# Kernel optimization log

Measured on AMD Instinct MI355X. Metric: run time of the kernel, lower is better.

The kernel has to match this reference:

```python
import jax, jax.numpy as jnp
import numpy as np

N = 50000      # nodes
E = 1600000    # edges (before self loops)
F = 128        # input_dim
H = 4          # num_heads
D = 32         # hidden_dim (per head)
B = 16         # graphs in batch
NEG_SLOPE = 0.2  # PyG GATv2Conv default negative_slope


def setup_inputs() -> dict:
    key = jax.random.key(0)
    ks = jax.random.split(key, 8)
    x = jax.random.normal(ks[0], (N, F), dtype=jnp.float32)
    edge_index = jax.random.randint(ks[1], (2, E), 0, N, dtype=jnp.int32)
    batch = jnp.sort(jax.random.randint(ks[2], (N,), 0, B, dtype=jnp.int32))
    s = 0.05
    W_l = jax.random.normal(ks[3], (F, H * D), dtype=jnp.float32) * s
    b_l = jnp.zeros((H * D,), dtype=jnp.float32)
    W_r = jax.random.normal(ks[4], (F, H * D), dtype=jnp.float32) * s
    b_r = jnp.zeros((H * D,), dtype=jnp.float32)
    att = jax.random.normal(ks[5], (H, D), dtype=jnp.float32) * s
    bias = jnp.zeros((H * D,), dtype=jnp.float32)
    return {"x": x, "edge_index": edge_index, "batch": batch,
            "W_l": W_l, "b_l": b_l, "W_r": W_r, "b_r": b_r,
            "att": att, "bias": bias}


def reference(x, edge_index, batch, W_l, b_l, W_r, b_r, att, bias):
    n = x.shape[0]
    # PyG GATv2Conv adds self loops by default
    loops = jnp.arange(n, dtype=edge_index.dtype)
    src = jnp.concatenate([edge_index[0], loops])  # message source j
    dst = jnp.concatenate([edge_index[1], loops])  # message target i

    xl = (x @ W_l + b_l).reshape(n, H, D)  # source transform
    xr = (x @ W_r + b_r).reshape(n, H, D)  # target transform

    # per-edge GATv2 attention logits: a^T LeakyReLU(xl_j + xr_i)
    m = xl[src] + xr[dst]                                   # [E+N, H, D]
    e = jnp.sum(jax.nn.leaky_relu(m, NEG_SLOPE) * att, -1)  # [E+N, H]

    # softmax over incoming edges of each destination node
    e_max = jax.ops.segment_max(e, dst, num_segments=n)
    ex = jnp.exp(e - e_max[dst])
    den = jax.ops.segment_sum(ex, dst, num_segments=n)
    alpha = ex / den[dst]                                   # [E+N, H]

    # weighted scatter-sum aggregation of source features
    out = jax.ops.segment_sum(alpha[..., None] * xl[src], dst, num_segments=n)
    out = out.reshape(n, H * D) + bias                      # concat heads + bias
    out = jax.nn.relu(out)

    # global max pool over nodes of each graph
    pooled = jax.ops.segment_max(out, batch, num_segments=B)
    pooled = jnp.where(jnp.isfinite(pooled), pooled, 0.0)   # guard empty graphs
    return pooled
```

## Files before the change

kernel.cpp:

```cpp
#include <hip/hip_runtime.h>

#define NN 50000
#define NE 1600000
#define FDIM 128
#define CDIM 128
#define NGRAPH 16
#define SLOPE 0.2f
#define CSTRIDE 96
#define BINSH 7
#define NBIN 391
#define EPB 6400
#define NB1 250
#define EPT 25
#define CAP 5120
#define POOL_NODES 64
#define POOL_NB ((NN + POOL_NODES - 1) / POOL_NODES)
#define TNB 782

__device__ __forceinline__ unsigned short f2bf(float f) {
    unsigned u = __float_as_uint(f);
    return (unsigned short)((u + 0x7FFFu + ((u >> 16) & 1u)) >> 16);
}
__device__ __forceinline__ unsigned packbf(float a, float b) {
    return (unsigned)f2bf(a) | ((unsigned)f2bf(b) << 16);
}
__device__ __forceinline__ unsigned short f2h(float f) {
    union { _Float16 h; unsigned short u; } c;
    c.h = (_Float16)f;
    return c.u;
}

typedef __attribute__((ext_vector_type(8))) short short8;
typedef __attribute__((ext_vector_type(4))) float f32x4;
typedef _Float16 h2 __attribute__((ext_vector_type(2)));
union FragU { uint4 u; short8 s; };
union HU    { uint4 u; h2 h[4]; };

__global__ __launch_bounds__(256) void k_init(float* __restrict__ out,
                                              int* __restrict__ gbin_cnt) {
    int i = blockIdx.x * 256 + threadIdx.x;
    if (i < NGRAPH * CDIM) out[i] = 0.f;
    if (i < NBIN) gbin_cnt[i] = 0;
}

__global__ __launch_bounds__(256) void k_front(
    const float* __restrict__ x,
    const float* __restrict__ Wl, const float* __restrict__ bl,
    const float* __restrict__ Wr, const float* __restrict__ br,
    const int* __restrict__ src, const int* __restrict__ dst,
    int* __restrict__ gbin_cnt, unsigned* __restrict__ gstage,
    unsigned short* __restrict__ xlh, unsigned short* __restrict__ xrh) {
    __shared__ __align__(16) char shraw[32768];
    const int tid = threadIdx.x;

    if (blockIdx.x < NB1) {
        int* bcnt = (int*)shraw;
        int* boff = bcnt + NBIN;
        int* gb   = boff + NBIN;
        int* sc   = gb + NBIN;
        unsigned* st = (unsigned*)(sc + 256);
        const int t  = tid;
        const int e0 = blockIdx.x * EPB;

        for (int b = t; b < NBIN; b += 256) bcnt[b] = 0;
        __syncthreads();

        unsigned sd[EPT]; int bn[EPT]; int pl[EPT];
#pragma unroll
        for (int k = 0; k < EPT; k++) {
            int e = e0 + k * 256 + t;
            int s = src[e], d = dst[e];
            bn[k] = d >> BINSH;
            sd[k] = (unsigned)s | ((unsigned)(d & 127) << 16)
                                | ((unsigned)bn[k] << 23);
            pl[k] = atomicAdd(&bcnt[bn[k]], 1);
        }
        __syncthreads();

        int c0 = (2*t     < NBIN) ? bcnt[2*t]     : 0;
        int c1 = (2*t + 1 < NBIN) ? bcnt[2*t + 1] : 0;
        int v  = c0 + c1;
        sc[t] = v; __syncthreads();
        for (int off = 1; off < 256; off <<= 1) {
            int add = (t >= off) ? sc[t - off] : 0;
            __syncthreads();
            sc[t] += add;
            __syncthreads();
        }
        int base = sc[t] - v;
        if (2*t     < NBIN) boff[2*t]     = base;
        if (2*t + 1 < NBIN) boff[2*t + 1] = base + c0;
        __syncthreads();

        for (int b = t; b < NBIN; b += 256) {
            int c = bcnt[b];
            gb[b] = (c > 0) ? atomicAdd(&gbin_cnt[b], c) : 0;
        }
#pragma unroll
        for (int k = 0; k < EPT; k++) st[boff[bn[k]] + pl[k]] = sd[k];
        __syncthreads();

        for (int idx = t; idx < EPB; idx += 256) {
            unsigned w = st[idx];
            int b = w >> 23;
            int p = gb[b] + (idx - boff[b]);
            if (p < CAP) gstage[(size_t)b * CAP + p] = w;
        }
    } else {
        uint4* wfrag = (uint4*)shraw;
        const int bid   = blockIdx.x - NB1;
        const int wv    = tid >> 6;
        const int lane  = tid & 63;
        const int quad  = lane >> 4;
        const int col   = lane & 15;
        const int node0 = bid * 64;
        const int nodeA = node0 + wv * 16 + col;
        const bool aval = nodeA < NN;

        FragU afrag[4];
#pragma unroll
        for (int kq = 0; kq < 4; kq++) {
            float4 lo = make_float4(0.f,0.f,0.f,0.f), hi = lo;
            if (aval) {
                const float* ap = &x[(size_t)nodeA * FDIM + kq * 32 + quad * 8];
                lo = *(const float4*)ap;
                hi = *(const float4*)(ap + 4);
            }
            afrag[kq].u.x = packbf(lo.x, lo.y);
            afrag[kq].u.y = packbf(lo.z, lo.w);
            afrag[kq].u.z = packbf(hi.x, hi.y);
            afrag[kq].u.w = packbf(hi.z, hi.w);
        }

        const int myrow0 = node0 + wv * 16 + quad * 4;

        for (int mat = 0; mat < 2; mat++) {
            const float* W  = mat ? Wr : Wl;
            const float* bb = mat ? br : bl;
            unsigned short* dsto = mat ? xrh : xlh;
            __syncthreads();
            for (int i = 0; i < 8; i++) {
                int C = i * 256 + tid;
                int ccol = C & 15, cq = (C >> 4) & 3, ckq = (C >> 6) & 3, cnt_ = C >> 8;
                const float* wp = &W[(size_t)(ckq * 32 + cq * 8) * CDIM + cnt_ * 16 + ccol];
                uint4 u;
                u.x = packbf(wp[0],        wp[CDIM]);
                u.y = packbf(wp[2*CDIM],   wp[3*CDIM]);
                u.z = packbf(wp[4*CDIM],   wp[5*CDIM]);
                u.w = packbf(wp[6*CDIM],   wp[7*CDIM]);
                wfrag[C] = u;
            }
            __syncthreads();

#pragma unroll
            for (int nt = 0; nt < 8; nt++) {
                f32x4 acc = {0.f, 0.f, 0.f, 0.f};
#pragma unroll
                for (int kq = 0; kq < 4; kq++) {
                    FragU bfr;
                    bfr.u = wfrag[(nt * 4 + kq) * 64 + lane];
                    acc = __builtin_amdgcn_mfma_f32_16x16x32_bf16(
                              afrag[kq].s, bfr.s, acc, 0, 0, 0);
                }
                int ch = nt * 16 + col;
                float bv = bb[ch];
#pragma unroll
                for (int r = 0; r < 4; r++) {
                    int node = myrow0 + r;
                    if (node < NN)
                        dsto[(size_t)node * CDIM + ch] = f2h(acc[r] + bv);
                }
            }
        }
    }
}

__global__ __launch_bounds__(512) void k_csr(
    const int* __restrict__ gbin_cnt, const unsigned* __restrict__ gstage,
    int* __restrict__ cnt, unsigned short* __restrict__ colp) {
    __shared__ int nfill[128];
    __shared__ unsigned short crow[128 * CSTRIDE];
    const int bin = blockIdx.x;
    const int t   = threadIdx.x;
    const int n0  = bin << BINSH;
    const int nb  = min(128, NN - n0);
    const int m   = min(gbin_cnt[bin], CAP);

    if (t < 128) nfill[t] = 0;
    __syncthreads();

    unsigned w[10];
    bool     ok[10];
#pragma unroll
    for (int k = 0; k < 10; k++) {
        int i = k * 512 + t;
        ok[k] = i < m;
        if (ok[k]) w[k] = gstage[(size_t)bin * CAP + i];
    }
#pragma unroll
    for (int k = 0; k < 10; k++) {
        if (ok[k]) {
            int dl = (w[k] >> 16) & 127;
            int p  = atomicAdd(&nfill[dl], 1);
            if (p < CSTRIDE - 1)
                crow[dl * CSTRIDE + p] = (unsigned short)(w[k] & 0xFFFF);
        }
    }
    __syncthreads();

    if (t < nb) {
        int c = min(nfill[t], CSTRIDE - 1);
        crow[t * CSTRIDE + c] = (unsigned short)(n0 + t);
        cnt[n0 + t] = c + 1;
    }
    __syncthreads();

    unsigned* gout = (unsigned*)colp + (size_t)bin * (128 * CSTRIDE / 2);
    const unsigned* cin = (const unsigned*)crow;
    for (int idx = t; idx < 128 * CSTRIDE / 2; idx += 512) gout[idx] = cin[idx];
}

__device__ __forceinline__ void edge_body(
    const char* __restrict__ xlb, unsigned chb, int j,
    const h2* __restrict__ rx, const h2* __restrict__ ah,
    float& s, float* __restrict__ acc) {
    HU q;
    q.u = *(const uint4*)(xlb + (((unsigned)j << 8) | chb));
    const h2 c02 = {(_Float16)SLOPE, (_Float16)SLOPE};
    float d = 0.f;
#pragma unroll
    for (int k = 0; k < 4; k++) {
        h2 t  = q.h[k] + rx[k];
        h2 lk = __builtin_elementwise_max(t, t * c02);
#if __has_builtin(__builtin_amdgcn_fdot2)
        d = __builtin_amdgcn_fdot2(lk, ah[k], d, false);
#else
        d = fmaf((float)lk.x, (float)ah[k].x, d);
        d = fmaf((float)lk.y, (float)ah[k].y, d);
#endif
    }
    d += __shfl_xor(d, 1);
    d += __shfl_xor(d, 2);
    float w = __expf(d);
    s += w;
#pragma unroll
    for (int k = 0; k < 4; k++) {
        acc[2*k]   = fmaf(w, (float)q.h[k].x, acc[2*k]);
        acc[2*k+1] = fmaf(w, (float)q.h[k].y, acc[2*k+1]);
    }
}

__global__ __launch_bounds__(256) void k_aggregate(
    const unsigned short* __restrict__ xlh, const unsigned short* __restrict__ xrh,
    const float* __restrict__ att, const float* __restrict__ bias,
    const int* __restrict__ cnt, const unsigned short* __restrict__ colp,
    float* __restrict__ nodeout) {
    const int wave = blockIdx.x * 4 + (threadIdx.x >> 6);
    const int lane = threadIdx.x & 63;
    const int i     = wave;
    const size_t start = (size_t)i * CSTRIDE;
    const int deg   = cnt[i];
    const int grp   = lane >> 4;
    const int ch0   = (lane & 15) * 8;
    const unsigned chb = (unsigned)(ch0 * 2);
    const char* xlb = (const char*)xlh;

    int cj0 = (int)colp[start + lane];
    int cj1 = 0;
    if (deg > 64) cj1 = (int)colp[start + 64 + lane];

    HU rxu;
    rxu.u = *(const uint4*)&xrh[(size_t)i * CDIM + ch0];
    const float4 aa0 = *(const float4*)&att[ch0];
    const float4 aa1 = *(const float4*)&att[ch0 + 4];
    h2 ah[4];
    ah[0] = h2{(_Float16)aa0.x, (_Float16)aa0.y};
    ah[1] = h2{(_Float16)aa0.z, (_Float16)aa0.w};
    ah[2] = h2{(_Float16)aa1.x, (_Float16)aa1.y};
    ah[3] = h2{(_Float16)aa1.z, (_Float16)aa1.w};

    float s = 0.f;
    float acc[8];
#pragma unroll
    for (int k = 0; k < 8; k++) acc[k] = 0.f;

    const int full = deg >> 2;
    const int f0   = full < 16 ? full : 16;
#pragma unroll 2
    for (int t = 0; t < f0; t++) {
        int j = __shfl(cj0, t * 4 + grp);
        edge_body(xlb, chb, j, rxu.h, ah, s, acc);
    }
    for (int t = 16; t < full; t++) {
        int j = __shfl(cj1, t * 4 + grp - 64);
        edge_body(xlb, chb, j, rxu.h, ah, s, acc);
    }
    int e  = full * 4 + grp;
    int jt = (e < 64) ? __shfl(cj0, e) : __shfl(cj1, (e - 64) & 63);
    if (e < deg)
        edge_body(xlb, chb, jt, rxu.h, ah, s, acc);

#pragma unroll
    for (int dist = 16; dist <= 32; dist <<= 1) {
        s += __shfl_xor(s, dist);
#pragma unroll
        for (int k = 0; k < 8; k++) acc[k] += __shfl_xor(acc[k], dist);
    }

    if (grp == 0) {
        float inv = 1.f / s;
        float4 o0, o1;
        const float4 b0 = *(const float4*)&bias[ch0];
        const float4 b1 = *(const float4*)&bias[ch0 + 4];
        o0.x = fmaxf(fmaf(acc[0], inv, b0.x), 0.f);
        o0.y = fmaxf(fmaf(acc[1], inv, b0.y), 0.f);
        o0.z = fmaxf(fmaf(acc[2], inv, b0.z), 0.f);
        o0.w = fmaxf(fmaf(acc[3], inv, b0.w), 0.f);
        o1.x = fmaxf(fmaf(acc[4], inv, b1.x), 0.f);
        o1.y = fmaxf(fmaf(acc[5], inv, b1.y), 0.f);
        o1.z = fmaxf(fmaf(acc[6], inv, b1.z), 0.f);
        o1.w = fmaxf(fmaf(acc[7], inv, b1.w), 0.f);
        float* op = &nodeout[(size_t)i * CDIM + ch0];
        *(float4*)op       = o0;
        *(float4*)(op + 4) = o1;
    }
}

__global__ __launch_bounds__(256) void k_pool(
    const float* __restrict__ nodeout, const int* __restrict__ batch,
    float* __restrict__ out) {
    const int tid  = threadIdx.x;
    const int c4   = (tid & 31) * 4;
    const int nl   = tid >> 5;
    const int base = blockIdx.x * POOL_NODES;
    float4 mx = make_float4(0.f, 0.f, 0.f, 0.f);
    int cur = -1;
#pragma unroll
    for (int k = 0; k < POOL_NODES / 8; k++) {
        int node = base + k * 8 + nl;
        if (node >= NN) break;
        int g = batch[node];
        if (g != cur) {
            if (cur >= 0) {
                int* op = (int*)&out[cur * CDIM + c4];
                if (mx.x > 0.f) atomicMax(op,     __float_as_int(mx.x));
                if (mx.y > 0.f) atomicMax(op + 1, __float_as_int(mx.y));
                if (mx.z > 0.f) atomicMax(op + 2, __float_as_int(mx.z));
                if (mx.w > 0.f) atomicMax(op + 3, __float_as_int(mx.w));
            }
            cur = g;
            mx = make_float4(0.f, 0.f, 0.f, 0.f);
        }
        float4 v = *(const float4*)&nodeout[(size_t)node * CDIM + c4];
        mx.x = fmaxf(mx.x, v.x);
        mx.y = fmaxf(mx.y, v.y);
        mx.z = fmaxf(mx.z, v.z);
        mx.w = fmaxf(mx.w, v.w);
    }
    if (cur >= 0) {
        int* op = (int*)&out[cur * CDIM + c4];
        if (mx.x > 0.f) atomicMax(op,     __float_as_int(mx.x));
        if (mx.y > 0.f) atomicMax(op + 1, __float_as_int(mx.y));
        if (mx.z > 0.f) atomicMax(op + 2, __float_as_int(mx.z));
        if (mx.w > 0.f) atomicMax(op + 3, __float_as_int(mx.w));
    }
}

extern "C" void kernel_launch(void* const* d_in, const int* in_sizes, int n_in,
                              void* d_out, int out_size, void* d_ws, size_t ws_size,
                              hipStream_t stream) {
    const float* x     = (const float*)d_in[0];
    const int*   ei    = (const int*)d_in[1];
    const int*   batch = (const int*)d_in[2];
    const float* Wl    = (const float*)d_in[3];
    const float* bl    = (const float*)d_in[4];
    const float* Wr    = (const float*)d_in[5];
    const float* br    = (const float*)d_in[6];
    const float* att   = (const float*)d_in[7];
    const float* bias  = (const float*)d_in[8];
    float* out = (float*)d_out;

    char* w = (char*)d_ws;
    float*          nodeout  = (float*)w;          w += (size_t)NN * CDIM * 4;
    unsigned short* xlh      = (unsigned short*)w; w += (size_t)NN * CDIM * 2;
    unsigned short* xrh      = (unsigned short*)w; w += (size_t)NN * CDIM * 2;
    int*            cnt      = (int*)w;            w += (size_t)NN * 4;
    unsigned short* colp     = (unsigned short*)w; w += (size_t)NBIN * 128 * CSTRIDE * 2;
    unsigned*       gstage   = (unsigned*)w;       w += (size_t)NBIN * CAP * 4;
    int*            gbin_cnt = (int*)w;            w += (size_t)NBIN * 4;

    const int* src = ei;
    const int* dst = ei + NE;

    k_init<<<10, 256, 0, stream>>>(out, gbin_cnt);
    k_front<<<NB1 + TNB, 256, 0, stream>>>(x, Wl, bl, Wr, br,
                                           src, dst, gbin_cnt, gstage, xlh, xrh);
    k_csr<<<NBIN, 512, 0, stream>>>(gbin_cnt, gstage, cnt, colp);
    k_aggregate<<<NN / 4, 256, 0, stream>>>(xlh, xrh, att, bias,
                                            cnt, colp, nodeout);
    k_pool<<<POOL_NB, 256, 0, stream>>>(nodeout, batch, out);
}
```

Measured before the change: 235.5 us.

## Prepack bf16 weights once, prefetch neighbor rows, use DPP quad reductions

```diff
diff --git a/kernel.cpp b/kernel.cpp
--- a/kernel.cpp
+++ b/kernel.cpp
@@ -36,20 +36,54 @@
 union FragU { uint4 u; short8 s; };
 union HU    { uint4 u; h2 h[4]; };
 
-__global__ __launch_bounds__(256) void k_init(float* __restrict__ out,
-                                              int* __restrict__ gbin_cnt) {
-    int i = blockIdx.x * 256 + threadIdx.x;
-    if (i < NGRAPH * CDIM) out[i] = 0.f;
-    if (i < NBIN) gbin_cnt[i] = 0;
+__device__ __forceinline__ float qadd_xor1(float d) {
+#if __has_builtin(__builtin_amdgcn_update_dpp)
+    int x = __builtin_amdgcn_update_dpp(0, __float_as_int(d), 0xB1, 0xF, 0xF, true);
+    return d + __int_as_float(x);
+#else
+    return d + __shfl_xor(d, 1);
+#endif
+}
+__device__ __forceinline__ float qadd_xor2(float d) {
+#if __has_builtin(__builtin_amdgcn_update_dpp)
+    int x = __builtin_amdgcn_update_dpp(0, __float_as_int(d), 0x4E, 0xF, 0xF, true);
+    return d + __int_as_float(x);
+#else
+    return d + __shfl_xor(d, 2);
+#endif
+}
+
+__global__ __launch_bounds__(256) void k_init(
+    float* __restrict__ out, int* __restrict__ gbin_cnt,
+    const float* __restrict__ Wl, const float* __restrict__ Wr,
+    uint4* __restrict__ wpack) {
+    const int b = blockIdx.x;
+    if (b < 16) {
+        int C = b * 256 + threadIdx.x;
+        const float* W = (C < 2048) ? Wl : Wr;
+        int c = C & 2047;
+        int ccol = c & 15, cq = (c >> 4) & 3, ckq = (c >> 6) & 3, cnt_ = c >> 8;
+        const float* wp = &W[(size_t)(ckq * 32 + cq * 8) * CDIM + cnt_ * 16 + ccol];
+        uint4 u;
+        u.x = packbf(wp[0],        wp[CDIM]);
+        u.y = packbf(wp[2*CDIM],   wp[3*CDIM]);
+        u.z = packbf(wp[4*CDIM],   wp[5*CDIM]);
+        u.w = packbf(wp[6*CDIM],   wp[7*CDIM]);
+        wpack[C] = u;
+    } else {
+        int i = (b - 16) * 256 + threadIdx.x;
+        if (i < NGRAPH * CDIM) out[i] = 0.f;
+        if (i < NBIN) gbin_cnt[i] = 0;
+    }
 }
 
 __global__ __launch_bounds__(256) void k_front(
     const float* __restrict__ x,
-    const float* __restrict__ Wl, const float* __restrict__ bl,
-    const float* __restrict__ Wr, const float* __restrict__ br,
+    const float* __restrict__ bl, const float* __restrict__ br,
     const int* __restrict__ src, const int* __restrict__ dst,
     int* __restrict__ gbin_cnt, unsigned* __restrict__ gstage,
-    unsigned short* __restrict__ xlh, unsigned short* __restrict__ xrh) {
+    unsigned short* __restrict__ xlh, unsigned short* __restrict__ xrh,
+    const uint4* __restrict__ wpack) {
     __shared__ __align__(16) char shraw[32768];
     const int tid = threadIdx.x;
 
@@ -135,21 +169,13 @@
         const int myrow0 = node0 + wv * 16 + quad * 4;
 
         for (int mat = 0; mat < 2; mat++) {
-            const float* W  = mat ? Wr : Wl;
             const float* bb = mat ? br : bl;
             unsigned short* dsto = mat ? xrh : xlh;
+            const uint4* wsrc = wpack + mat * 2048;
             __syncthreads();
-            for (int i = 0; i < 8; i++) {
-                int C = i * 256 + tid;
-                int ccol = C & 15, cq = (C >> 4) & 3, ckq = (C >> 6) & 3, cnt_ = C >> 8;
-                const float* wp = &W[(size_t)(ckq * 32 + cq * 8) * CDIM + cnt_ * 16 + ccol];
-                uint4 u;
-                u.x = packbf(wp[0],        wp[CDIM]);
-                u.y = packbf(wp[2*CDIM],   wp[3*CDIM]);
-                u.z = packbf(wp[4*CDIM],   wp[5*CDIM]);
-                u.w = packbf(wp[6*CDIM],   wp[7*CDIM]);
-                wfrag[C] = u;
-            }
+#pragma unroll
+            for (int i = 0; i < 8; i++)
+                wfrag[i * 256 + tid] = wsrc[i * 256 + tid];
             __syncthreads();
 
 #pragma unroll
@@ -220,12 +246,11 @@
     for (int idx = t; idx < 128 * CSTRIDE / 2; idx += 512) gout[idx] = cin[idx];
 }
 
-__device__ __forceinline__ void edge_body(
-    const char* __restrict__ xlb, unsigned chb, int j,
+__device__ __forceinline__ void edge_compute(
+    uint4 qu,
     const h2* __restrict__ rx, const h2* __restrict__ ah,
     float& s, float* __restrict__ acc) {
-    HU q;
-    q.u = *(const uint4*)(xlb + (((unsigned)j << 8) | chb));
+    HU q; q.u = qu;
     const h2 c02 = {(_Float16)SLOPE, (_Float16)SLOPE};
     float d = 0.f;
 #pragma unroll
@@ -239,8 +264,8 @@
         d = fmaf((float)lk.y, (float)ah[k].y, d);
 #endif
     }
-    d += __shfl_xor(d, 1);
-    d += __shfl_xor(d, 2);
+    d = qadd_xor1(d);
+    d = qadd_xor2(d);
     float w = __expf(d);
     s += w;
 #pragma unroll
@@ -248,6 +273,14 @@
         acc[2*k]   = fmaf(w, (float)q.h[k].x, acc[2*k]);
         acc[2*k+1] = fmaf(w, (float)q.h[k].y, acc[2*k+1]);
     }
+}
+
+__device__ __forceinline__ void edge_body(
+    const char* __restrict__ xlb, unsigned chb, int j,
+    const h2* __restrict__ rx, const h2* __restrict__ ah,
+    float& s, float* __restrict__ acc) {
+    uint4 qu = *(const uint4*)(xlb + (((unsigned)j << 8) | chb));
+    edge_compute(qu, rx, ah, s, acc);
 }
 
 __global__ __launch_bounds__(256) void k_aggregate(
@@ -286,10 +319,24 @@
 
     const int full = deg >> 2;
     const int f0   = full < 16 ? full : 16;
-#pragma unroll 2
-    for (int t = 0; t < f0; t++) {
-        int j = __shfl(cj0, t * 4 + grp);
-        edge_body(xlb, chb, j, rxu.h, ah, s, acc);
+
+    if (f0 > 0) {
+        int ja = __shfl(cj0, grp);
+        uint4 qa = *(const uint4*)(xlb + (((unsigned)ja << 8) | chb));
+        if (f0 > 1) {
+            int jb = __shfl(cj0, 4 + grp);
+            uint4 qb = *(const uint4*)(xlb + (((unsigned)jb << 8) | chb));
+            for (int t = 0; t + 2 < f0; t++) {
+                int jc = __shfl(cj0, (t + 2) * 4 + grp);
+                uint4 qc = *(const uint4*)(xlb + (((unsigned)jc << 8) | chb));
+                edge_compute(qa, rxu.h, ah, s, acc);
+                qa = qb; qb = qc;
+            }
+            edge_compute(qa, rxu.h, ah, s, acc);
+            edge_compute(qb, rxu.h, ah, s, acc);
+        } else {
+            edge_compute(qa, rxu.h, ah, s, acc);
+        }
     }
     for (int t = 16; t < full; t++) {
         int j = __shfl(cj1, t * 4 + grp - 64);
@@ -388,13 +435,15 @@
     unsigned short* colp     = (unsigned short*)w; w += (size_t)NBIN * 128 * CSTRIDE * 2;
     unsigned*       gstage   = (unsigned*)w;       w += (size_t)NBIN * CAP * 4;
     int*            gbin_cnt = (int*)w;            w += (size_t)NBIN * 4;
+    uint4*          wpack    = (uint4*)w;          w += (size_t)4096 * 16;
 
     const int* src = ei;
     const int* dst = ei + NE;
 
-    k_init<<<10, 256, 0, stream>>>(out, gbin_cnt);
-    k_front<<<NB1 + TNB, 256, 0, stream>>>(x, Wl, bl, Wr, br,
-                                           src, dst, gbin_cnt, gstage, xlh, xrh);
+    k_init<<<26, 256, 0, stream>>>(out, gbin_cnt, Wl, Wr, wpack);
+    k_front<<<NB1 + TNB, 256, 0, stream>>>(x, bl, br,
+                                           src, dst, gbin_cnt, gstage, xlh, xrh,
+                                           wpack);
     k_csr<<<NBIN, 512, 0, stream>>>(gbin_cnt, gstage, cnt, colp);
     k_aggregate<<<NN / 4, 256, 0, stream>>>(xlh, xrh, att, bias,
                                             cnt, colp, nodeout);
```

After: 225.7 us. -4.2%, faster.
